# Optimization experiments

Hardware: AMD Instinct MI355X
Metric: run time of the kernel (lower is better)

Reference implementation:

```python
import jax, jax.numpy as jnp
import numpy as np

BM = 64; BN = 64          # block_m, block_n
NKM = BM // 4; NKN = BN // 4   # tokens sampled per block (16)
# topk_newtype bands: cumulative-pooled-attention fraction -> granularity value (0 = skip block)
RATIO_BANDS = [(1, 0.05), (2, 0.15), (4, 0.25), (8, 0.5)]


def setup_inputs() -> dict:
    key = jax.random.key(0)
    kq, kk, kv, ki, kj = jax.random.split(key, 5)
    B, H, L, D = 1, 8, 4096, 64
    q = jax.random.normal(kq, (B, H, L, D), jnp.float32)
    k = jax.random.normal(kk, (B, H, L, D), jnp.float32)
    v = jax.random.normal(kv, (B, H, L, D), jnp.float32)
    # distinct in-block sample positions, shared across blocks per (B,H)
    # (mirrors torch.topk(torch.rand(B,H,1,block), sample_num))
    sample_idx_q = jnp.argsort(jax.random.uniform(ki, (B, H, BM)), axis=-1)[..., :NKM].astype(jnp.int32)
    sample_idx_k = jnp.argsort(jax.random.uniform(kj, (B, H, BN)), axis=-1)[..., :NKN].astype(jnp.int32)
    return {"q": q, "k": k, "v": v, "sample_idx_q": sample_idx_q, "sample_idx_k": sample_idx_k}


def _sample_blocks(x, idx, bs, nk):
    # x: [B,H,L,D]; idx: [B,H,nk] in-block positions -> [B,H,nb*nk,D]
    B, H, L, D = x.shape
    nb = L // bs
    xb = x.reshape(B, H, nb, bs, D)
    gidx = jnp.broadcast_to(idx[:, :, None, :, None], (B, H, nb, nk, D))
    return jnp.take_along_axis(xb, gidx, axis=3).reshape(B, H, nb * nk, D)


def _block_mask(q, k, sample_idx_q, sample_idx_k):
    # pooled downsampled attention -> per-(q_block,k_block) keep mask (topk_newtype)
    B, H, L, D = q.shape
    qb, kb = L // BM, L // BN
    sq = _sample_blocks(q, sample_idx_q, BM, NKM)  # [B,H,qb*NKM,D]
    sk = _sample_blocks(k, sample_idx_k, BN, NKN)  # [B,H,kb*NKN,D]
    scores = jnp.einsum('bhqd,bhkd->bhqk', sq, sk) / jnp.sqrt(jnp.float32(D))
    attn = jax.nn.softmax(scores, axis=-1)
    # NKM x NKN sum-pooling == block-level pooled attention mass  [B,H,qb,kb]
    pooling = attn.reshape(B, H, qb, NKM, kb, NKN).sum(axis=(3, 5))
    # rank key-blocks per q-block row by pooled mass, band by cumulative fraction
    order = jnp.argsort(-pooling, axis=-1)
    sp = jnp.take_along_axis(pooling, order, axis=-1)
    cs = jnp.cumsum(sp, axis=-1)
    frac_before = (cs - sp) / cs[..., -1:]
    val = jnp.zeros_like(sp)
    for g, hi in RATIO_BANDS[::-1]:
        val = jnp.where(frac_before < hi, jnp.float32(g), val)
    rank = jnp.argsort(order, axis=-1)          # inverse permutation
    mask_vals = jnp.take_along_axis(val, rank, axis=-1)  # [B,H,qb,kb] in {0,1,2,4,8}
    return mask_vals > 0


def reference(q, k, v, sample_idx_q, sample_idx_k):
    B, H, L, D = q.shape
    attend = _block_mask(q, k, sample_idx_q, sample_idx_k)            # [B,H,qb,kb]
    attend_tok = jnp.repeat(jnp.repeat(attend, BM, axis=2), BN, axis=3)  # [B,H,L,L]
    scores = jnp.einsum('bhqd,bhkd->bhqk', q, k) / jnp.sqrt(jnp.float32(D))
    scores = jnp.where(attend_tok, scores, jnp.float32(-1e30))
    p = jax.nn.softmax(scores, axis=-1)
    return jnp.einsum('bhqk,bhkd->bhqd', p, v)
```

## Files before the change

kernel.cpp:

```cpp
#include <hip/hip_runtime.h>
#include <hip/hip_bf16.h>

#define H_ 8
#define L_ 4096
#define D_ 64
#define NB_ 64

typedef __attribute__((ext_vector_type(8))) short bf16x8;
typedef __attribute__((ext_vector_type(4))) float f32x4;

__device__ __forceinline__ unsigned short f2bf(float x) {
    unsigned u = __float_as_uint(x);
    u += 0x7fff + ((u >> 16) & 1);
    return (unsigned short)(u >> 16);
}
__device__ __forceinline__ float bf2f(unsigned short s) {
    return __uint_as_float(((unsigned)s) << 16);
}
__device__ __forceinline__ void gload_lds16(const unsigned short* g, unsigned short* l) {
    __builtin_amdgcn_global_load_lds(
        (const __attribute__((address_space(1))) unsigned int*)(const void*)g,
        (__attribute__((address_space(3))) unsigned int*)(void*)l,
        16, 0, 0);
}

__global__ __launch_bounds__(256) void prep_kernel(
    const float* __restrict__ q, const float* __restrict__ k, const float* __restrict__ v,
    const int* __restrict__ sidxk,
    unsigned short* __restrict__ qhi, unsigned short* __restrict__ qlo,
    unsigned short* __restrict__ khi,
    unsigned short* __restrict__ vth,
    unsigned short* __restrict__ skh, unsigned short* __restrict__ skl)
{
    const int h  = blockIdx.x >> 6;
    const int tb = blockIdx.x & 63;
    const int tid = threadIdx.x;
    __shared__ float vst[64][68];

    const size_t te = ((size_t)(h*64 + tb)) << 12;
    const float4* qg = (const float4*)(q + te);
    for (int i4 = tid; i4 < 1024; i4 += 256) {
        float4 t = qg[i4];
        ushort4 hi, lo;
        hi.x = f2bf(t.x); lo.x = f2bf(t.x - bf2f(hi.x));
        hi.y = f2bf(t.y); lo.y = f2bf(t.y - bf2f(hi.y));
        hi.z = f2bf(t.z); lo.z = f2bf(t.z - bf2f(hi.z));
        hi.w = f2bf(t.w); lo.w = f2bf(t.w - bf2f(hi.w));
        *(ushort4*)(qhi + te + i4*4) = hi;
        *(ushort4*)(qlo + te + i4*4) = lo;
    }
    const float4* kg = (const float4*)(k + te);
    for (int i4 = tid; i4 < 1024; i4 += 256) {
        float4 t = kg[i4];
        int r = i4 >> 4, c4 = i4 & 15;
        int sch = (c4 >> 1) ^ ((r >> 2) & 7);
        ushort4 hi;
        hi.x = f2bf(t.x); hi.y = f2bf(t.y); hi.z = f2bf(t.z); hi.w = f2bf(t.w);
        *(ushort4*)(khi + te + r*64 + sch*8 + (c4 & 1)*4) = hi;
    }
    {
        int t = tid >> 4, d4 = tid & 15;
        int srow = tb*64 + sidxk[h*16 + t];
        float4 x = *(const float4*)(k + ((size_t)h*L_ + srow)*D_ + d4*4);
        ushort4 hi, lo;
        hi.x = f2bf(x.x); lo.x = f2bf(x.x - bf2f(hi.x));
        hi.y = f2bf(x.y); lo.y = f2bf(x.y - bf2f(hi.y));
        hi.z = f2bf(x.z); lo.z = f2bf(x.z - bf2f(hi.z));
        hi.w = f2bf(x.w); lo.w = f2bf(x.w - bf2f(hi.w));
        int sch = (d4 >> 1) ^ (t & 7);
        size_t dst = ((size_t)h*1024 + tb*16 + t)*64 + sch*8 + (d4 & 1)*4;
        *(ushort4*)(skh + dst) = hi;
        *(ushort4*)(skl + dst) = lo;
    }
    const float4* vg = (const float4*)(v + te);
    for (int i4 = tid; i4 < 1024; i4 += 256) {
        float4 t = vg[i4];
        *(float4*)&vst[i4 >> 4][(i4 & 15)*4] = t;
    }
    __syncthreads();
    for (int u = tid; u < 512; u += 256) {
        int d = u >> 3, kc8 = u & 7;
        int sch = kc8 ^ (d & 7);
        ushort4 h0, h1;
        h0.x = f2bf(vst[kc8*8+0][d]); h0.y = f2bf(vst[kc8*8+1][d]);
        h0.z = f2bf(vst[kc8*8+2][d]); h0.w = f2bf(vst[kc8*8+3][d]);
        h1.x = f2bf(vst[kc8*8+4][d]); h1.y = f2bf(vst[kc8*8+5][d]);
        h1.z = f2bf(vst[kc8*8+6][d]); h1.w = f2bf(vst[kc8*8+7][d]);
        *(ushort4*)(vth + te + d*64 + sch*8 + 0) = h0;
        *(ushort4*)(vth + te + d*64 + sch*8 + 4) = h1;
    }
}

__global__ __launch_bounds__(256, 4) void mask_mfma(
    const unsigned short* __restrict__ qhi, const unsigned short* __restrict__ qlo,
    const unsigned short* __restrict__ skh, const unsigned short* __restrict__ skl,
    const int* __restrict__ sidxq,
    unsigned long long* __restrict__ maskbits)
{
    const int h    = blockIdx.x & 7;
    const int qb   = blockIdx.x >> 3;
    const int tid  = threadIdx.x;
    const int wave = tid >> 6;
    const int lane = tid & 63;
    const int l16  = lane & 15;
    const int quad = lane >> 4;

    __shared__ __align__(16) unsigned short ch[8192];
    __shared__ __align__(16) unsigned short cl[8192];
    __shared__ float E[16][64];
    __shared__ float Z[16];
    __shared__ float pooled[64];

    for (int e = tid; e < 16*64; e += 256) (&E[0][0])[e] = 0.f;

    const int iqr = sidxq[h*16 + l16];
    const size_t qo = (((size_t)(h*64 + qb)) << 12) + (size_t)iqr*64;
    bf16x8 qh[2], ql[2];
    qh[0] = *(const bf16x8*)(qhi + qo + quad*8);
    qh[1] = *(const bf16x8*)(qhi + qo + 32 + quad*8);
    ql[0] = *(const bf16x8*)(qlo + qo + quad*8);
    ql[1] = *(const bf16x8*)(qlo + qo + 32 + quad*8);
    __syncthreads();

    for (int cc = 0; cc < 8; ++cc) {
        const bf16x8* gh = (const bf16x8*)(skh + ((size_t)h*1024 + cc*128)*64);
        const bf16x8* gl = (const bf16x8*)(skl + ((size_t)h*1024 + cc*128)*64);
        for (int i = tid; i < 1024; i += 256) {
            ((bf16x8*)ch)[i] = gh[i];
            ((bf16x8*)cl)[i] = gl[i];
        }
        __syncthreads();

        #pragma unroll
        for (int tt = 0; tt < 2; ++tt) {
            const int kb = cc*8 + wave*2 + tt;
            const int nb = (wave*2 + tt)*16;
            f32x4 sacc = (f32x4){0.f, 0.f, 0.f, 0.f};
            #pragma unroll
            for (int kc = 0; kc < 2; ++kc) {
                const int off = (nb + l16)*64 + (((kc*4 + quad) ^ (l16 & 7))*8);
                bf16x8 kh = *(const bf16x8*)&ch[off];
                bf16x8 kl = *(const bf16x8*)&cl[off];
                sacc = __builtin_amdgcn_mfma_f32_16x16x32_bf16(qh[kc], kh, sacc, 0, 0, 0);
                sacc = __builtin_amdgcn_mfma_f32_16x16x32_bf16(qh[kc], kl, sacc, 0, 0, 0);
                sacc = __builtin_amdgcn_mfma_f32_16x16x32_bf16(ql[kc], kh, sacc, 0, 0, 0);
                sacc = __builtin_amdgcn_mfma_f32_16x16x32_bf16(ql[kc], kl, sacc, 0, 0, 0);
            }
            #pragma unroll
            for (int r = 0; r < 4; ++r) {
                float p = __expf(sacc[r] * 0.125f);
                p += __shfl_xor(p, 1);
                p += __shfl_xor(p, 2);
                p += __shfl_xor(p, 4);
                p += __shfl_xor(p, 8);
                if (l16 == 0) E[quad*4 + r][kb] = p;
            }
        }
        __syncthreads();
    }

    if (tid < 16) {
        float s = 0.f;
        #pragma unroll
        for (int kb = 0; kb < 64; ++kb) s += E[tid][kb];
        Z[tid] = s;
    }
    __syncthreads();
    if (tid < 64) {
        float s = 0.f;
        #pragma unroll
        for (int t = 0; t < 16; ++t) s += E[t][tid] / Z[t];
        pooled[tid] = s;
    }
    __syncthreads();
    if (tid < 64) {
        float pi = pooled[tid];
        float tot = 0.f, bef = 0.f;
        for (int j2 = 0; j2 < 64; ++j2) {
            float pj = pooled[j2];
            tot += pj;
            if (pj > pi || (pj == pi && j2 < tid)) bef += pj;
        }
        bool att = (bef / tot) < 0.5f;
        unsigned long long bits = __ballot(att);
        if (tid == 0) maskbits[h*64 + qb] = bits;
    }
}

__global__ __launch_bounds__(256, 2) void attn_fast(
    const unsigned short* __restrict__ qhi, const unsigned short* __restrict__ qlo,
    const unsigned short* __restrict__ khi,
    const unsigned short* __restrict__ vth,
    const unsigned long long* __restrict__ maskbits,
    float* __restrict__ out)
{
    const int h    = blockIdx.x & 7;
    const int qb   = blockIdx.x >> 3;
    const int tid  = threadIdx.x;
    const int wave = tid >> 6;
    const int lane = tid & 63;
    const int l16  = lane & 15;
    const int quad = lane >> 4;

    __shared__ __align__(16) unsigned short bufK[2][4096];
    __shared__ __align__(16) unsigned short bufVh[2][4096];
    __shared__ __align__(16) unsigned short ps[4][16][88];

    const size_t qoff = (((size_t)(h*64 + qb)) << 12) + (size_t)(wave*16 + l16)*64;
    bf16x8 qfh[2], qfl[2];
    qfh[0] = *(const bf16x8*)(qhi + qoff + quad*8);
    qfh[1] = *(const bf16x8*)(qhi + qoff + 32 + quad*8);
    qfl[0] = *(const bf16x8*)(qlo + qoff + quad*8);
    qfl[1] = *(const bf16x8*)(qlo + qoff + 32 + quad*8);

    const unsigned long long bm = maskbits[(h << 6) + qb];

    float lpart[4];
    f32x4 oacc[4];
    #pragma unroll
    for (int r = 0; r < 4; ++r) lpart[r] = 0.f;
    #pragma unroll
    for (int t = 0; t < 4; ++t) oacc[t] = (f32x4){0.f, 0.f, 0.f, 0.f};

    auto dma_stage = [&](int kb, int b) {
        const size_t tb = ((size_t)(h*64 + kb)) << 12;
        gload_lds16(khi + tb + tid*8,         &bufK [b][tid*8]);
        gload_lds16(khi + tb + (tid+256)*8,   &bufK [b][(tid+256)*8]);
        gload_lds16(vth + tb + tid*8,         &bufVh[b][tid*8]);
        gload_lds16(vth + tb + (tid+256)*8,   &bufVh[b][(tid+256)*8]);
    };

    auto compute = [&](int b) {
        f32x4 sacc[4];
        #pragma unroll
        for (int t = 0; t < 4; ++t) sacc[t] = (f32x4){0.f, 0.f, 0.f, 0.f};
        #pragma unroll
        for (int t = 0; t < 4; ++t) {
            #pragma unroll
            for (int kc = 0; kc < 2; ++kc) {
                bf16x8 kf = *(const bf16x8*)&bufK[b][(l16*4 + t)*64 + (((kc*4 + quad) ^ (l16 & 7))*8)];
                sacc[t] = __builtin_amdgcn_mfma_f32_16x16x32_bf16(qfh[kc], kf, sacc[t], 0, 0, 0);
                sacc[t] = __builtin_amdgcn_mfma_f32_16x16x32_bf16(qfl[kc], kf, sacc[t], 0, 0, 0);
            }
        }
        #pragma unroll
        for (int r = 0; r < 4; ++r) {
            float p0 = __expf(fmaf(sacc[0][r], 0.125f, -16.0f));
            float p1 = __expf(fmaf(sacc[1][r], 0.125f, -16.0f));
            float p2 = __expf(fmaf(sacc[2][r], 0.125f, -16.0f));
            float p3 = __expf(fmaf(sacc[3][r], 0.125f, -16.0f));
            __hip_bfloat162 a01 = __float22bfloat162_rn(make_float2(p0, p1));
            __hip_bfloat162 a23 = __float22bfloat162_rn(make_float2(p2, p3));
            unsigned u01 = *(unsigned*)&a01;
            unsigned u23 = *(unsigned*)&a23;
            uint2 w; w.x = u01; w.y = u23;
            *(uint2*)&ps[wave][quad*4 + r][l16*4] = w;
            lpart[r] += (bf2f((unsigned short)(u01 & 0xffffu)) + bf2f((unsigned short)(u01 >> 16)))
                      + (bf2f((unsigned short)(u23 & 0xffffu)) + bf2f((unsigned short)(u23 >> 16)));
        }
        bf16x8 pf[2];
        #pragma unroll
        for (int kc = 0; kc < 2; ++kc)
            pf[kc] = *(const bf16x8*)&ps[wave][l16][kc*32 + quad*8];
        #pragma unroll
        for (int t = 0; t < 4; ++t) {
            #pragma unroll
            for (int kc = 0; kc < 2; ++kc) {
                bf16x8 vh = *(const bf16x8*)&bufVh[b][(t*16 + l16)*64 + (((kc*4 + quad) ^ (l16 & 7))*8)];
                oacc[t] = __builtin_amdgcn_mfma_f32_16x16x32_bf16(pf[kc], vh, oacc[t], 0, 0, 0);
            }
        }
    };

    unsigned long long rem = bm;
    int cur = 0;
    {
        int kb0 = (int)__builtin_ctzll(rem); rem &= rem - 1;
        dma_stage(kb0, 0);
    }
    for (;;) {
        __syncthreads();
        int nxt = -1;
        if (rem) { nxt = (int)__builtin_ctzll(rem); rem &= rem - 1; dma_stage(nxt, cur ^ 1); }
        compute(cur);
        if (nxt < 0) break;
        cur ^= 1;
    }

    #pragma unroll
    for (int off = 1; off < 16; off <<= 1)
        #pragma unroll
        for (int r = 0; r < 4; ++r)
            lpart[r] += __shfl_xor(lpart[r], off);

    float* og = out + ((size_t)h*L_ + (size_t)qb*64)*D_ + (size_t)(wave*16 + quad*4)*D_;
    #pragma unroll
    for (int r = 0; r < 4; ++r) {
        float inv = 1.f / lpart[r];
        #pragma unroll
        for (int t = 0; t < 4; ++t)
            og[(size_t)r*D_ + t*16 + l16] = oacc[t][r] * inv;
    }
}

__global__ __launch_bounds__(256, 4) void mask_kernel4(
    const float* __restrict__ q, const float* __restrict__ k,
    const int* __restrict__ sidxq, const int* __restrict__ sidxk,
    unsigned long long* __restrict__ maskbits)
{
    const int h   = blockIdx.x >> 6;
    const int qb  = blockIdx.x & 63;
    const int tid = threadIdx.x;
    const int rg  = tid >> 5;
    const int cg  = tid & 31;

    __shared__ float sq[16][68];
    __shared__ float skc[128][68];
    __shared__ float E[16][64];
    __shared__ float Z[16];
    __shared__ float pooled[64];
    __shared__ int iq[16], ik[16];

    if (tid < 16) { iq[tid] = sidxq[h*16 + tid]; ik[tid] = sidxk[h*16 + tid]; }
    for (int e = tid; e < 16*64; e += 256) (&E[0][0])[e] = 0.f;
    __syncthreads();
    {
        int j = tid >> 4, d4 = tid & 15;
        int grow = h*L_ + qb*64 + iq[j];
        *(float4*)&sq[j][d4*4] = *(const float4*)(q + (size_t)grow*D_ + d4*4);
    }
    for (int cc = 0; cc < 8; ++cc) {
        for (int i = tid; i < 2048; i += 256) {
            int col = i >> 4, d4 = i & 15;
            int colg = cc*128 + col;
            int grow = h*L_ + (colg >> 4)*64 + ik[colg & 15];
            *(float4*)&skc[col][d4*4] = *(const float4*)(k + (size_t)grow*D_ + d4*4);
        }
        __syncthreads();
        float acc[2][4] = {{0.f,0.f,0.f,0.f},{0.f,0.f,0.f,0.f}};
        #pragma unroll 4
        for (int d4 = 0; d4 < 16; ++d4) {
            float4 qv0 = *(const float4*)&sq[rg*2 + 0][d4*4];
            float4 qv1 = *(const float4*)&sq[rg*2 + 1][d4*4];
            #pragma unroll
            for (int j = 0; j < 4; ++j) {
                float4 kv = *(const float4*)&skc[cg + 32*j][d4*4];
                acc[0][j] += qv0.x*kv.x + qv0.y*kv.y + qv0.z*kv.z + qv0.w*kv.w;
                acc[1][j] += qv1.x*kv.x + qv1.y*kv.y + qv1.z*kv.z + qv1.w*kv.w;
            }
        }
        #pragma unroll
        for (int j = 0; j < 4; ++j) {
            int kb = cc*8 + (cg >> 4) + 2*j;
            #pragma unroll
            for (int i = 0; i < 2; ++i) {
                float p = __expf(acc[i][j] * 0.125f);
                p += __shfl_xor(p, 1);
                p += __shfl_xor(p, 2);
                p += __shfl_xor(p, 4);
                p += __shfl_xor(p, 8);
                if ((cg & 15) == 0) E[rg*2 + i][kb] += p;
            }
        }
        __syncthreads();
    }
    if (tid < 16) {
        float s = 0.f;
        #pragma unroll
        for (int kb = 0; kb < 64; ++kb) s += E[tid][kb];
        Z[tid] = s;
    }
    __syncthreads();
    if (tid < 64) {
        float s = 0.f;
        #pragma unroll
        for (int t = 0; t < 16; ++t) s += E[t][tid] / Z[t];
        pooled[tid] = s;
    }
    __syncthreads();
    if (tid < 64) {
        float pi = pooled[tid];
        float tot = 0.f, bef = 0.f;
        for (int j2 = 0; j2 < 64; ++j2) {
            float pj = pooled[j2];
            tot += pj;
            if (pj > pi || (pj == pi && j2 < tid)) bef += pj;
        }
        bool att = (bef / tot) < 0.5f;
        unsigned long long bits = __ballot(att);
        if (tid == 0) maskbits[h*64 + qb] = bits;
    }
}

__global__ __launch_bounds__(256, 3) void attn_v3(
    const float* __restrict__ q, const float* __restrict__ k, const float* __restrict__ v,
    const unsigned long long* __restrict__ maskbits, float* __restrict__ out)
{
    const int h = blockIdx.x >> 6, qb = blockIdx.x & 63;
    const int tid = threadIdx.x, wave = tid >> 6, lane = tid & 63;
    const int l16 = lane & 15, quad = lane >> 4;
    __shared__ __align__(16) unsigned short ks_hi[64][72];
    __shared__ __align__(16) unsigned short ks_lo[64][72];
    __shared__ __align__(16) unsigned short vt_hi[64][72];
    __shared__ __align__(16) unsigned short vt_lo[64][72];
    __shared__ __align__(16) unsigned short ps[4][16][72];

    const float4* qg = (const float4*)(q + ((size_t)h*L_ + (size_t)qb*64)*D_);
    for (int i4 = tid; i4 < 1024; i4 += 256) {
        float4 t = qg[i4];
        int r = i4 >> 4, c = (i4 & 15) << 2;
        ushort4 hi, lo;
        hi.x = f2bf(t.x); lo.x = f2bf(t.x - bf2f(hi.x));
        hi.y = f2bf(t.y); lo.y = f2bf(t.y - bf2f(hi.y));
        hi.z = f2bf(t.z); lo.z = f2bf(t.z - bf2f(hi.z));
        hi.w = f2bf(t.w); lo.w = f2bf(t.w - bf2f(hi.w));
        *(ushort4*)&ks_hi[r][c] = hi;
        *(ushort4*)&ks_lo[r][c] = lo;
    }
    const unsigned long long bm = maskbits[(h << 6) + qb];
    __syncthreads();
    bf16x8 qhi2[2], qlo2[2];
    #pragma unroll
    for (int kc = 0; kc < 2; ++kc) {
        qhi2[kc] = *(const bf16x8*)&ks_hi[wave*16 + l16][kc*32 + quad*8];
        qlo2[kc] = *(const bf16x8*)&ks_lo[wave*16 + l16][kc*32 + quad*8];
    }
    __syncthreads();
    float m_i[4], l_i[4];
    f32x4 oacc[4];
    #pragma unroll
    for (int r = 0; r < 4; ++r) { m_i[r] = -1e30f; l_i[r] = 0.f; }
    #pragma unroll
    for (int t = 0; t < 4; ++t) oacc[t] = (f32x4){0.f, 0.f, 0.f, 0.f};
    for (int kb = 0; kb < 64; ++kb) {
        if (!((bm >> kb) & 1ull)) continue;
        const float4* kg = (const float4*)(k + ((size_t)h*L_ + (size_t)kb*64)*D_);
        const float*  vg = v + ((size_t)h*L_ + (size_t)kb*64)*D_;
        for (int i4 = tid; i4 < 1024; i4 += 256) {
            float4 t = kg[i4];
            int r = i4 >> 4, c = (i4 & 15) << 2;
            ushort4 hi, lo;
            hi.x = f2bf(t.x); lo.x = f2bf(t.x - bf2f(hi.x));
            hi.y = f2bf(t.y); lo.y = f2bf(t.y - bf2f(hi.y));
            hi.z = f2bf(t.z); lo.z = f2bf(t.z - bf2f(hi.z));
            hi.w = f2bf(t.w); lo.w = f2bf(t.w - bf2f(hi.w));
            *(ushort4*)&ks_hi[r][c] = hi;
            *(ushort4*)&ks_lo[r][c] = lo;
        }
        for (int tsk = tid; tsk < 512; tsk += 256) {
            int rp = tsk >> 4;
            int c  = (tsk & 15) << 2;
            float4 a0 = *(const float4*)(vg + (size_t)(2*rp)*D_ + c);
            float4 a1 = *(const float4*)(vg + (size_t)(2*rp+1)*D_ + c);
            #pragma unroll
            for (int j = 0; j < 4; ++j) {
                float x0 = (j==0)?a0.x:(j==1)?a0.y:(j==2)?a0.z:a0.w;
                float x1 = (j==0)?a1.x:(j==1)?a1.y:(j==2)?a1.z:a1.w;
                unsigned short h0 = f2bf(x0), h1b = f2bf(x1);
                *(unsigned*)&vt_hi[c+j][2*rp] = (unsigned)h0 | ((unsigned)h1b << 16);
                unsigned short lo0 = f2bf(x0 - bf2f(h0)), lo1 = f2bf(x1 - bf2f(h1b));
                *(unsigned*)&vt_lo[c+j][2*rp] = (unsigned)lo0 | ((unsigned)lo1 << 16);
            }
        }
        __syncthreads();
        f32x4 sacc[4];
        #pragma unroll
        for (int t = 0; t < 4; ++t) sacc[t] = (f32x4){0.f, 0.f, 0.f, 0.f};
        #pragma unroll
        for (int t = 0; t < 4; ++t) {
            #pragma unroll
            for (int kc = 0; kc < 2; ++kc) {
                bf16x8 khi2 = *(const bf16x8*)&ks_hi[t*16 + l16][kc*32 + quad*8];
                bf16x8 klo2 = *(const bf16x8*)&ks_lo[t*16 + l16][kc*32 + quad*8];
                sacc[t] = __builtin_amdgcn_mfma_f32_16x16x32_bf16(qhi2[kc], khi2, sacc[t], 0, 0, 0);
                sacc[t] = __builtin_amdgcn_mfma_f32_16x16x32_bf16(qhi2[kc], klo2, sacc[t], 0, 0, 0);
                sacc[t] = __builtin_amdgcn_mfma_f32_16x16x32_bf16(qlo2[kc], khi2, sacc[t], 0, 0, 0);
            }
        }
        #pragma unroll
        for (int t = 0; t < 4; ++t) sacc[t] *= 0.125f;
        float rowmax[4];
        #pragma unroll
        for (int r = 0; r < 4; ++r)
            rowmax[r] = fmaxf(fmaxf(sacc[0][r], sacc[1][r]), fmaxf(sacc[2][r], sacc[3][r]));
        #pragma unroll
        for (int off = 1; off < 16; off <<= 1)
            #pragma unroll
            for (int r = 0; r < 4; ++r)
                rowmax[r] = fmaxf(rowmax[r], __shfl_xor(rowmax[r], off));
        float al[4], rs[4];
        #pragma unroll
        for (int r = 0; r < 4; ++r) {
            float mnew = fmaxf(m_i[r], rowmax[r]);
            al[r] = __expf(m_i[r] - mnew);
            m_i[r] = mnew;
            float acc = 0.f;
            #pragma unroll
            for (int t = 0; t < 4; ++t) {
                float p = __expf(sacc[t][r] - mnew);
                unsigned short pb = f2bf(p);
                ps[wave][quad*4 + r][t*16 + l16] = pb;
                acc += bf2f(pb);
            }
            rs[r] = acc;
        }
        #pragma unroll
        for (int off = 1; off < 16; off <<= 1)
            #pragma unroll
            for (int r = 0; r < 4; ++r)
                rs[r] += __shfl_xor(rs[r], off);
        #pragma unroll
        for (int r = 0; r < 4; ++r) l_i[r] = l_i[r] * al[r] + rs[r];
        #pragma unroll
        for (int t = 0; t < 4; ++t)
            #pragma unroll
            for (int r = 0; r < 4; ++r) oacc[t][r] *= al[r];
        bf16x8 pf[2];
        #pragma unroll
        for (int kc = 0; kc < 2; ++kc)
            pf[kc] = *(const bf16x8*)&ps[wave][l16][kc*32 + quad*8];
        #pragma unroll
        for (int t = 0; t < 4; ++t) {
            #pragma unroll
            for (int kc = 0; kc < 2; ++kc) {
                bf16x8 vhif = *(const bf16x8*)&vt_hi[t*16 + l16][kc*32 + quad*8];
                bf16x8 vlof = *(const bf16x8*)&vt_lo[t*16 + l16][kc*32 + quad*8];
                oacc[t] = __builtin_amdgcn_mfma_f32_16x16x32_bf16(pf[kc], vhif, oacc[t], 0, 0, 0);
                oacc[t] = __builtin_amdgcn_mfma_f32_16x16x32_bf16(pf[kc], vlof, oacc[t], 0, 0, 0);
            }
        }
        __syncthreads();
    }
    float* og = out + ((size_t)h*L_ + (size_t)qb*64)*D_ + (size_t)(wave*16 + quad*4)*D_;
    #pragma unroll
    for (int r = 0; r < 4; ++r) {
        float inv = 1.f / l_i[r];
        #pragma unroll
        for (int t = 0; t < 4; ++t)
            og[(size_t)r*D_ + t*16 + l16] = oacc[t][r] * inv;
    }
}

extern "C" void kernel_launch(void* const* d_in, const int* in_sizes, int n_in,
                              void* d_out, int out_size, void* d_ws, size_t ws_size,
                              hipStream_t stream) {
    const float* q = (const float*)d_in[0];
    const float* k = (const float*)d_in[1];
    const float* v = (const float*)d_in[2];
    const int* siq = (const int*)d_in[3];
    const int* sik = (const int*)d_in[4];
    float* out = (float*)d_out;

    char* ws = (char*)d_ws;
    unsigned long long* mask = (unsigned long long*)ws;
    const size_t TEN = (size_t)H_*L_*D_;
    const size_t SKN = (size_t)H_*1024*64;
    unsigned short* qhi = (unsigned short*)(ws + 4096);
    unsigned short* qlo = qhi + TEN;
    unsigned short* khi = qlo + TEN;
    unsigned short* vth = khi + TEN;
    unsigned short* skh = vth + TEN;
    unsigned short* skl = skh + SKN;
    const size_t need = 4096 + (4*TEN + 2*SKN)*sizeof(unsigned short);

    if (ws_size >= need) {
        prep_kernel<<<dim3(H_*NB_), dim3(256), 0, stream>>>(q, k, v, sik, qhi, qlo, khi, vth, skh, skl);
        mask_mfma<<<dim3(H_*NB_), dim3(256), 0, stream>>>(qhi, qlo, skh, skl, siq, mask);
        attn_fast<<<dim3(H_*NB_), dim3(256), 0, stream>>>(qhi, qlo, khi, vth, mask, out);
    } else {
        mask_kernel4<<<dim3(H_*NB_), dim3(256), 0, stream>>>(q, k, siq, sik, mask);
        attn_v3<<<dim3(H_*NB_), dim3(256), 0, stream>>>(q, k, v, mask, out);
    }
}
```

Before: 146.7 us.

## Split attended key blocks across waves with register-held K/V and LDS reduction

The attention kernel now stages the whole 64-row Q tile in swizzled LDS. Each of the four waves takes every fourth attended key block, loading K and V straight from global memory into registers with a one-block prefetch, which removes the shared LDS double-buffer and the per-iteration block-wide barriers. Each wave keeps partial outputs and row sums for all 64 query rows, and these are reduced through LDS at the end. The exponential is switched to a native exp2 with the scale folded in. In exchange the kernel holds far more registers per wave, uses about 65 KB of LDS, and adds a final cross-wave reduction, all of which may reduce occupancy.

```diff
diff --git a/kernel.cpp b/kernel.cpp
--- a/kernel.cpp
+++ b/kernel.cpp
@@ -187,7 +187,7 @@
     }
 }
 
-__global__ __launch_bounds__(256, 2) void attn_fast(
+__global__ __launch_bounds__(256, 2) void attn_wave(
     const unsigned short* __restrict__ qhi, const unsigned short* __restrict__ qlo,
     const unsigned short* __restrict__ khi,
     const unsigned short* __restrict__ vth,
@@ -202,104 +202,163 @@
     const int l16  = lane & 15;
     const int quad = lane >> 4;
 
-    __shared__ __align__(16) unsigned short bufK[2][4096];
-    __shared__ __align__(16) unsigned short bufVh[2][4096];
-    __shared__ __align__(16) unsigned short ps[4][16][88];
-
-    const size_t qoff = (((size_t)(h*64 + qb)) << 12) + (size_t)(wave*16 + l16)*64;
-    bf16x8 qfh[2], qfl[2];
-    qfh[0] = *(const bf16x8*)(qhi + qoff + quad*8);
-    qfh[1] = *(const bf16x8*)(qhi + qoff + 32 + quad*8);
-    qfl[0] = *(const bf16x8*)(qlo + qoff + quad*8);
-    qfl[1] = *(const bf16x8*)(qlo + qoff + 32 + quad*8);
-
-    const unsigned long long bm = maskbits[(h << 6) + qb];
-
-    float lpart[4];
-    f32x4 oacc[4];
-    #pragma unroll
-    for (int r = 0; r < 4; ++r) lpart[r] = 0.f;
-    #pragma unroll
-    for (int t = 0; t < 4; ++t) oacc[t] = (f32x4){0.f, 0.f, 0.f, 0.f};
-
-    auto dma_stage = [&](int kb, int b) {
-        const size_t tb = ((size_t)(h*64 + kb)) << 12;
-        gload_lds16(khi + tb + tid*8,         &bufK [b][tid*8]);
-        gload_lds16(khi + tb + (tid+256)*8,   &bufK [b][(tid+256)*8]);
-        gload_lds16(vth + tb + tid*8,         &bufVh[b][tid*8]);
-        gload_lds16(vth + tb + (tid+256)*8,   &bufVh[b][(tid+256)*8]);
-    };
-
-    auto compute = [&](int b) {
-        f32x4 sacc[4];
-        #pragma unroll
-        for (int t = 0; t < 4; ++t) sacc[t] = (f32x4){0.f, 0.f, 0.f, 0.f};
-        #pragma unroll
-        for (int t = 0; t < 4; ++t) {
+    __shared__ __align__(16) char SM[66560];
+    unsigned short* Qh = (unsigned short*)SM;
+    unsigned short* Ql = (unsigned short*)(SM + 9216);
+    unsigned short* ps = (unsigned short*)(SM + 18432 + wave*11264);
+
+    const size_t qbase = ((size_t)(h*64 + qb)) << 12;
+
+    for (int c = tid; c < 512; c += 256) {
+        int row = c >> 3, cc = c & 7;
+        int sw = cc ^ ((row >> 2) & 7);
+        uint4 th = *(const uint4*)(qhi + qbase + row*64 + cc*8);
+        uint4 tl = *(const uint4*)(qlo + qbase + row*64 + cc*8);
+        *(uint4*)&Qh[row*72 + sw*8] = th;
+        *(uint4*)&Ql[row*72 + sw*8] = tl;
+    }
+
+    unsigned long long rem = maskbits[(h << 6) + qb];
+    for (int s = 0; s < wave; ++s) rem &= rem - 1;
+    int cur = rem ? (int)__builtin_ctzll(rem) : -1;
+
+    float lp[4][4];
+    f32x4 oacc[4][4];
+    #pragma unroll
+    for (int qt = 0; qt < 4; ++qt)
+        #pragma unroll
+        for (int r = 0; r < 4; ++r) lp[qt][r] = 0.f;
+    #pragma unroll
+    for (int qt = 0; qt < 4; ++qt)
+        #pragma unroll
+        for (int dt = 0; dt < 4; ++dt) oacc[qt][dt] = (f32x4){0.f, 0.f, 0.f, 0.f};
+
+    bf16x8 kf[4][2], vf[4][2];
+    if (cur >= 0) {
+        const size_t tb = ((size_t)(h*64 + cur)) << 12;
+        #pragma unroll
+        for (int t = 0; t < 4; ++t)
             #pragma unroll
             for (int kc = 0; kc < 2; ++kc) {
-                bf16x8 kf = *(const bf16x8*)&bufK[b][(l16*4 + t)*64 + (((kc*4 + quad) ^ (l16 & 7))*8)];
-                sacc[t] = __builtin_amdgcn_mfma_f32_16x16x32_bf16(qfh[kc], kf, sacc[t], 0, 0, 0);
-                sacc[t] = __builtin_amdgcn_mfma_f32_16x16x32_bf16(qfl[kc], kf, sacc[t], 0, 0, 0);
-            }
-        }
-        #pragma unroll
-        for (int r = 0; r < 4; ++r) {
-            float p0 = __expf(fmaf(sacc[0][r], 0.125f, -16.0f));
-            float p1 = __expf(fmaf(sacc[1][r], 0.125f, -16.0f));
-            float p2 = __expf(fmaf(sacc[2][r], 0.125f, -16.0f));
-            float p3 = __expf(fmaf(sacc[3][r], 0.125f, -16.0f));
-            __hip_bfloat162 a01 = __float22bfloat162_rn(make_float2(p0, p1));
-            __hip_bfloat162 a23 = __float22bfloat162_rn(make_float2(p2, p3));
-            unsigned u01 = *(unsigned*)&a01;
-            unsigned u23 = *(unsigned*)&a23;
-            uint2 w; w.x = u01; w.y = u23;
-            *(uint2*)&ps[wave][quad*4 + r][l16*4] = w;
-            lpart[r] += (bf2f((unsigned short)(u01 & 0xffffu)) + bf2f((unsigned short)(u01 >> 16)))
-                      + (bf2f((unsigned short)(u23 & 0xffffu)) + bf2f((unsigned short)(u23 >> 16)));
-        }
-        bf16x8 pf[2];
-        #pragma unroll
-        for (int kc = 0; kc < 2; ++kc)
-            pf[kc] = *(const bf16x8*)&ps[wave][l16][kc*32 + quad*8];
-        #pragma unroll
-        for (int t = 0; t < 4; ++t) {
+                kf[t][kc] = *(const bf16x8*)(khi + tb + (l16*4 + t)*64 + (((kc*4 + quad) ^ (l16 & 7))*8));
+                vf[t][kc] = *(const bf16x8*)(vth + tb + (t*16 + l16)*64 + (((kc*4 + quad) ^ (l16 & 7))*8));
+            }
+    }
+    __syncthreads();
+
+    while (cur >= 0) {
+        rem &= rem - 1; rem &= rem - 1; rem &= rem - 1; rem &= rem - 1;
+        const int nxt = rem ? (int)__builtin_ctzll(rem) : -1;
+
+        #pragma unroll
+        for (int qt = 0; qt < 4; ++qt) {
+            const int xb = (qt*4 + (l16 >> 2)) & 7;
+            bf16x8 ah[2], al[2];
             #pragma unroll
             for (int kc = 0; kc < 2; ++kc) {
-                bf16x8 vh = *(const bf16x8*)&bufVh[b][(t*16 + l16)*64 + (((kc*4 + quad) ^ (l16 & 7))*8)];
-                oacc[t] = __builtin_amdgcn_mfma_f32_16x16x32_bf16(pf[kc], vh, oacc[t], 0, 0, 0);
-            }
-        }
-    };
-
-    unsigned long long rem = bm;
-    int cur = 0;
+                const int off = (qt*16 + l16)*72 + (((kc*4 + quad) ^ xb)*8);
+                ah[kc] = *(const bf16x8*)&Qh[off];
+                al[kc] = *(const bf16x8*)&Ql[off];
+            }
+            f32x4 sacc[4];
+            #pragma unroll
+            for (int t = 0; t < 4; ++t) sacc[t] = (f32x4){0.f, 0.f, 0.f, 0.f};
+            #pragma unroll
+            for (int t = 0; t < 4; ++t)
+                #pragma unroll
+                for (int kc = 0; kc < 2; ++kc) {
+                    sacc[t] = __builtin_amdgcn_mfma_f32_16x16x32_bf16(ah[kc], kf[t][kc], sacc[t], 0, 0, 0);
+                    sacc[t] = __builtin_amdgcn_mfma_f32_16x16x32_bf16(al[kc], kf[t][kc], sacc[t], 0, 0, 0);
+                }
+            #pragma unroll
+            for (int r = 0; r < 4; ++r) {
+                float p0 = __builtin_amdgcn_exp2f(fmaf(sacc[0][r], 0.18033688f, -23.083121f));
+                float p1 = __builtin_amdgcn_exp2f(fmaf(sacc[1][r], 0.18033688f, -23.083121f));
+                float p2 = __builtin_amdgcn_exp2f(fmaf(sacc[2][r], 0.18033688f, -23.083121f));
+                float p3 = __builtin_amdgcn_exp2f(fmaf(sacc[3][r], 0.18033688f, -23.083121f));
+                __hip_bfloat162 a01 = __float22bfloat162_rn(make_float2(p0, p1));
+                __hip_bfloat162 a23 = __float22bfloat162_rn(make_float2(p2, p3));
+                unsigned u01 = *(unsigned*)&a01;
+                unsigned u23 = *(unsigned*)&a23;
+                uint2 w; w.x = u01; w.y = u23;
+                *(uint2*)&ps[(qt*16 + quad*4 + r)*88 + l16*4] = w;
+                lp[qt][r] += (bf2f((unsigned short)(u01 & 0xffffu)) + bf2f((unsigned short)(u01 >> 16)))
+                           + (bf2f((unsigned short)(u23 & 0xffffu)) + bf2f((unsigned short)(u23 >> 16)));
+            }
+        }
+        if (nxt >= 0) {
+            const size_t tb = ((size_t)(h*64 + nxt)) << 12;
+            #pragma unroll
+            for (int t = 0; t < 4; ++t)
+                #pragma unroll
+                for (int kc = 0; kc < 2; ++kc)
+                    kf[t][kc] = *(const bf16x8*)(khi + tb + (l16*4 + t)*64 + (((kc*4 + quad) ^ (l16 & 7))*8));
+        }
+        #pragma unroll
+        for (int qt = 0; qt < 4; ++qt) {
+            bf16x8 pf0 = *(const bf16x8*)&ps[(qt*16 + l16)*88 + quad*8];
+            bf16x8 pf1 = *(const bf16x8*)&ps[(qt*16 + l16)*88 + 32 + quad*8];
+            #pragma unroll
+            for (int dt = 0; dt < 4; ++dt) {
+                oacc[qt][dt] = __builtin_amdgcn_mfma_f32_16x16x32_bf16(pf0, vf[dt][0], oacc[qt][dt], 0, 0, 0);
+                oacc[qt][dt] = __builtin_amdgcn_mfma_f32_16x16x32_bf16(pf1, vf[dt][1], oacc[qt][dt], 0, 0, 0);
+            }
+        }
+        if (nxt >= 0) {
+            const size_t tb = ((size_t)(h*64 + nxt)) << 12;
+            #pragma unroll
+            for (int dt = 0; dt < 4; ++dt)
+                #pragma unroll
+                for (int kc = 0; kc < 2; ++kc)
+                    vf[dt][kc] = *(const bf16x8*)(vth + tb + (dt*16 + l16)*64 + (((kc*4 + quad) ^ (l16 & 7))*8));
+        }
+        cur = nxt;
+    }
+
+    #pragma unroll
+    for (int off = 1; off < 16; off <<= 1)
+        #pragma unroll
+        for (int qt = 0; qt < 4; ++qt)
+            #pragma unroll
+            for (int r = 0; r < 4; ++r)
+                lp[qt][r] += __shfl_xor(lp[qt][r], off);
+
+    __syncthreads();
+    float* ored = (float*)SM;
+    float* lred = (float*)(SM + 65536);
+    #pragma unroll
+    for (int qt = 0; qt < 4; ++qt) {
+        #pragma unroll
+        for (int dt = 0; dt < 4; ++dt)
+            #pragma unroll
+            for (int r = 0; r < 4; ++r)
+                ored[wave*4096 + (qt*16 + quad*4 + r)*64 + dt*16 + l16] = oacc[qt][dt][r];
+        if (l16 == 0) {
+            #pragma unroll
+            for (int r = 0; r < 4; ++r)
+                lred[wave*64 + qt*16 + quad*4 + r] = lp[qt][r];
+        }
+    }
+    __syncthreads();
     {
-        int kb0 = (int)__builtin_ctzll(rem); rem &= rem - 1;
-        dma_stage(kb0, 0);
-    }
-    for (;;) {
-        __syncthreads();
-        int nxt = -1;
-        if (rem) { nxt = (int)__builtin_ctzll(rem); rem &= rem - 1; dma_stage(nxt, cur ^ 1); }
-        compute(cur);
-        if (nxt < 0) break;
-        cur ^= 1;
-    }
-
-    #pragma unroll
-    for (int off = 1; off < 16; off <<= 1)
-        #pragma unroll
-        for (int r = 0; r < 4; ++r)
-            lpart[r] += __shfl_xor(lpart[r], off);
-
-    float* og = out + ((size_t)h*L_ + (size_t)qb*64)*D_ + (size_t)(wave*16 + quad*4)*D_;
-    #pragma unroll
-    for (int r = 0; r < 4; ++r) {
-        float inv = 1.f / lpart[r];
-        #pragma unroll
-        for (int t = 0; t < 4; ++t)
-            og[(size_t)r*D_ + t*16 + l16] = oacc[t][r] * inv;
+        const int row = tid >> 2;
+        const int d0  = (tid & 3) << 4;
+        float l = lred[row] + lred[64 + row] + lred[128 + row] + lred[192 + row];
+        float inv = 1.f / l;
+        float* og = out + ((size_t)h*L_ + (size_t)qb*64 + row)*D_ + d0;
+        #pragma unroll
+        for (int j = 0; j < 16; j += 4) {
+            float4 a = *(float4*)&ored[0*4096 + row*64 + d0 + j];
+            float4 b = *(float4*)&ored[1*4096 + row*64 + d0 + j];
+            float4 c = *(float4*)&ored[2*4096 + row*64 + d0 + j];
+            float4 d = *(float4*)&ored[3*4096 + row*64 + d0 + j];
+            float4 rr;
+            rr.x = (a.x + b.x + c.x + d.x) * inv;
+            rr.y = (a.y + b.y + c.y + d.y) * inv;
+            rr.z = (a.z + b.z + c.z + d.z) * inv;
+            rr.w = (a.w + b.w + c.w + d.w) * inv;
+            *(float4*)(og + j) = rr;
+        }
     }
 }
 
@@ -566,7 +625,7 @@
     if (ws_size >= need) {
         prep_kernel<<<dim3(H_*NB_), dim3(256), 0, stream>>>(q, k, v, sik, qhi, qlo, khi, vth, skh, skl);
         mask_mfma<<<dim3(H_*NB_), dim3(256), 0, stream>>>(qhi, qlo, skh, skl, siq, mask);
-        attn_fast<<<dim3(H_*NB_), dim3(256), 0, stream>>>(qhi, qlo, khi, vth, mask, out);
+        attn_wave<<<dim3(H_*NB_), dim3(256), 0, stream>>>(qhi, qlo, khi, vth, mask, out);
     } else {
         mask_kernel4<<<dim3(H_*NB_), dim3(256), 0, stream>>>(q, k, siq, sik, mask);
         attn_v3<<<dim3(H_*NB_), dim3(256), 0, stream>>>(q, k, v, mask, out);
```

After: 140.6 us. 1.04x faster.
